# Kernel optimization log

Hardware: AMD Instinct MI355X
Metric: run time of the kernel (lower is better)

The kernel has to match this reference:

```python
import jax, jax.numpy as jnp
import numpy as np

B, T, V, E, U = 1024, 256, 50000, 512, 1024

def setup_inputs() -> dict:
    key = jax.random.key(0)
    ks = jax.random.split(key, 10)
    s = lambda k, shape, fan: jax.random.normal(k, shape, dtype=jnp.float32) * (1.0 / np.sqrt(fan))
    return {
        "inputs": jax.random.randint(ks[0], (B, T), 0, V, dtype=jnp.int32),
        "emb": s(ks[1], (V, E), E),
        "W0": s(ks[2], (E, U), E),
        "U0": s(ks[3], (U, U), U),
        "b0": jnp.zeros((U,), jnp.float32),
        "W1": s(ks[4], (U, U), U),
        "U1": s(ks[5], (U, U), U),
        "b1": jnp.zeros((U,), jnp.float32),
        "Wout": s(ks[6], (U, 1), U),
        "bout": jnp.zeros((1,), jnp.float32),
    }

def reference(inputs, emb, W0, U0, b0, W1, U1, b1, Wout, bout):
    x = emb[inputs]                      # [B, T, E] embedding lookup
    xT = jnp.swapaxes(x, 0, 1)           # [T, B, E] time-major for scan
    h0_init = jnp.zeros((inputs.shape[0], U0.shape[0]), x.dtype)
    h1_init = jnp.zeros((inputs.shape[0], U1.shape[0]), x.dtype)

    def step(carry, xt):
        h0, h1 = carry
        h0 = jnp.tanh(xt @ W0 + h0 @ U0 + b0)   # SimpleRNNCell 0 (dropout inactive, inference)
        h1 = jnp.tanh(h0 @ W1 + h1 @ U1 + b1)   # SimpleRNNCell 1
        return (h0, h1), None

    (h0, h1), _ = jax.lax.scan(step, (h0_init, h1_init), xT)
    return jax.nn.sigmoid(h1 @ Wout + bout)      # [B, 1]
```

## Files before the change

### kernel.cpp

```cpp
#include <hip/hip_runtime.h>
#include <hip/hip_cooperative_groups.h>
#include <math.h>

namespace cg = cooperative_groups;

typedef unsigned short u16;
typedef __bf16 bf16x8 __attribute__((ext_vector_type(8)));
typedef float f32x4 __attribute__((ext_vector_type(4)));
typedef unsigned short u16x8 __attribute__((ext_vector_type(8)));
typedef int i32x4 __attribute__((ext_vector_type(4)));

#define NBLK 256
#define NTHR 256
#define BB 1024
#define TT 256
#define EE 512
#define UU 1024
#define K0 1536
#define K1 2048
#define NK0 48
#define NK1 64
#define HN0 ((size_t)BB * K0)
#define HN1 ((size_t)BB * K1)
#define LDS_BYTES 131072

#define ROSTER_BASE 0
#define FLAG_BASE 32
#define EPOCH_BASE (32 + 2048)
#define BAR_INTS 2560

#define AUX_SC0 1

__device__ i32x4 llvm_amdgcn_raw_buffer_load_i32x4(i32x4 srsrc, int voffset, int soffset,
                                                   int aux) __asm("llvm.amdgcn.raw.buffer.load.v4i32");

__device__ __forceinline__ i32x4 make_srd(const void* p) {
  union { const void* p; int i[2]; } u; u.p = p;
  i32x4 r; r.x = u.i[0]; r.y = u.i[1]; r.z = -1; r.w = 0x00020000;
  return r;
}

__device__ __forceinline__ u16 f2bf(float f) {
  unsigned u = __builtin_bit_cast(unsigned, f);
  u += 0x7fffu + ((u >> 16) & 1u);
  return (u16)(u >> 16);
}
__device__ __forceinline__ float bf2f(u16 h) {
  return __builtin_bit_cast(float, ((unsigned)h) << 16);
}
__device__ __forceinline__ float fast_tanh(float x) {
  x = fminf(fmaxf(x, -15.f), 15.f);
  float e = __expf(2.f * x);
  return (e - 1.f) / (e + 1.f);
}

template<int K, int KLOW>
__device__ __forceinline__ void wfill(u16* __restrict__ Wt,
    const float* __restrict__ Wl, const float* __restrict__ Wh, int gstart) {
  constexpr int NK = K / 32;
  constexpr int NG = 1024 * K / 8;
  for (int g = gstart; g < NG; g += NBLK * NTHR) {
    const int lane = g & 63;
    const int r = g >> 6;
    const int kt = r % NK;
    const int cb = r / NK;
    const int n = cb * 16 + (lane & 15);
    const int kb = kt * 32 + (lane >> 4) * 8;
    u16x8 o;
#pragma unroll
    for (int e = 0; e < 8; ++e) {
      const int k = kb + e;
      const float v = (k < KLOW) ? Wl[(size_t)k * UU + n] : Wh[(size_t)(k - KLOW) * UU + n];
      o[e] = f2bf(v);
    }
    *(u16x8*)(Wt + (size_t)g * 8) = o;
  }
}

__device__ __forceinline__ void xbar(int* __restrict__ bar, int xcc, int slot, int nx,
                                     int tgt, int tid) {
  __syncthreads();
  if (tid < 64) {
    if (tid == 0)
      __hip_atomic_store(&bar[FLAG_BASE + xcc * 256 + slot], tgt,
                         __ATOMIC_RELAXED, __HIP_MEMORY_SCOPE_AGENT);
    if (slot == 0) {
      for (int base = 0; base < nx; base += 64) {
        const int i = base + tid;
        const bool act = (i < nx);
        int guard = 0;
        bool done = false;
        do {
          int v = act ? __hip_atomic_load(&bar[FLAG_BASE + xcc * 256 + i],
                                          __ATOMIC_RELAXED, __HIP_MEMORY_SCOPE_AGENT)
                      : tgt;
          done = __all(v >= tgt) != 0;
        } while (!done && ++guard < 300000);
      }
      if (tid == 0)
        __hip_atomic_store(&bar[EPOCH_BASE + xcc * 32], tgt,
                           __ATOMIC_RELAXED, __HIP_MEMORY_SCOPE_AGENT);
    } else if (tid == 0) {
      int guard = 0;
      while (__hip_atomic_load(&bar[EPOCH_BASE + xcc * 32],
                               __ATOMIC_RELAXED, __HIP_MEMORY_SCOPE_AGENT) < tgt
             && ++guard < 600000)
        __builtin_amdgcn_s_sleep(8);
    }
  }
  __syncthreads();
}

template<int K>
__device__ __forceinline__ void gemm2(const i32x4& srdA, int voA,
    const u16* __restrict__ bA, const u16* __restrict__ bB, int lane,
    f32x4 (&acc)[2][4]) {
  constexpr int NK = K / 32;
#pragma unroll 4
  for (int kt = 0; kt < NK; ++kt) {
    i32x4 a0 = llvm_amdgcn_raw_buffer_load_i32x4(srdA, voA + kt * 64, 0, AUX_SC0);
    i32x4 a1 = llvm_amdgcn_raw_buffer_load_i32x4(srdA, voA + 16 * K * 2 + kt * 64, 0, AUX_SC0);
    u16x8 b0 = *(const u16x8*)(bA + (size_t)(0 * NK + kt) * 512 + lane * 8);
    u16x8 b1 = *(const u16x8*)(bA + (size_t)(1 * NK + kt) * 512 + lane * 8);
    u16x8 b2 = *(const u16x8*)(bB + (size_t)(0 * NK + kt) * 512 + lane * 8);
    u16x8 b3 = *(const u16x8*)(bB + (size_t)(1 * NK + kt) * 512 + lane * 8);
    bf16x8 fa0 = __builtin_bit_cast(bf16x8, a0);
    bf16x8 fa1 = __builtin_bit_cast(bf16x8, a1);
    bf16x8 fb0 = __builtin_bit_cast(bf16x8, b0);
    bf16x8 fb1 = __builtin_bit_cast(bf16x8, b1);
    bf16x8 fb2 = __builtin_bit_cast(bf16x8, b2);
    bf16x8 fb3 = __builtin_bit_cast(bf16x8, b3);
    acc[0][0] = __builtin_amdgcn_mfma_f32_16x16x32_bf16(fa0, fb0, acc[0][0], 0, 0, 0);
    acc[0][1] = __builtin_amdgcn_mfma_f32_16x16x32_bf16(fa0, fb1, acc[0][1], 0, 0, 0);
    acc[0][2] = __builtin_amdgcn_mfma_f32_16x16x32_bf16(fa0, fb2, acc[0][2], 0, 0, 0);
    acc[0][3] = __builtin_amdgcn_mfma_f32_16x16x32_bf16(fa0, fb3, acc[0][3], 0, 0, 0);
    acc[1][0] = __builtin_amdgcn_mfma_f32_16x16x32_bf16(fa1, fb0, acc[1][0], 0, 0, 0);
    acc[1][1] = __builtin_amdgcn_mfma_f32_16x16x32_bf16(fa1, fb1, acc[1][1], 0, 0, 0);
    acc[1][2] = __builtin_amdgcn_mfma_f32_16x16x32_bf16(fa1, fb2, acc[1][2], 0, 0, 0);
    acc[1][3] = __builtin_amdgcn_mfma_f32_16x16x32_bf16(fa1, fb3, acc[1][3], 0, 0, 0);
  }
}

__device__ __forceinline__ void do_l0(int tk, int xcc, int jl, bool uselds,
    const u16* __restrict__ ldsb, const u16* __restrict__ Wt0,
    const int* __restrict__ inputs, const float* __restrict__ emb,
    const float* __restrict__ b0, u16* __restrict__ A0, u16* __restrict__ A1,
    int tid)
{
  const int lane = tid & 63, w = tid >> 6, q = lane >> 4, l16 = lane & 15;
  const int c0 = jl * 64;
  if (tk < TT - 1) {
    const int grow = xcc * 128 + jl * 8 + (tid >> 5);
    const int c = (tid & 31) * 16;
    const int idx = inputs[grow * TT + tk + 1];
    const f32x4* s = (const f32x4*)(emb + (size_t)idx * EE + c);
    f32x4 f0 = s[0], f1 = s[1], f2 = s[2], f3 = s[3];
    u16x8 oa, ob;
#pragma unroll
    for (int j = 0; j < 4; ++j) {
      oa[j] = f2bf(f0[j]); oa[j + 4] = f2bf(f1[j]);
      ob[j] = f2bf(f2[j]); ob[j + 4] = f2bf(f3[j]);
    }
    u16* dst = A0 + (size_t)((tk + 1) & 1) * HN0 + (size_t)grow * K0 + c;
    *(u16x8*)dst = oa;
    *(u16x8*)(dst + 8) = ob;
  }
  if (tk < TT) {
    f32x4 acc[2][4];
#pragma unroll
    for (int i = 0; i < 2; ++i)
#pragma unroll
      for (int n = 0; n < 4; ++n) acc[i][n] = (f32x4){0.f, 0.f, 0.f, 0.f};
    i32x4 srdA = make_srd(A0 + (size_t)(tk & 1) * HN0);
    const int voA = ((xcc * 128 + w * 32 + l16) * K0 + q * 8) * 2;
    const u16* bB = Wt0 + (size_t)(c0 / 16 + 2) * NK0 * 512;
    if (uselds) gemm2<K0>(srdA, voA, ldsb, bB, lane, acc);
    else        gemm2<K0>(srdA, voA, Wt0 + (size_t)(c0 / 16) * NK0 * 512, bB, lane, acc);
    u16* d1 = A1 + (size_t)(tk & 1) * HN1;
    u16* d2 = A0 + (size_t)((tk + 1) & 1) * HN0 + 512;
#pragma unroll
    for (int n = 0; n < 4; ++n) {
      const int col = c0 + n * 16 + l16;
      const float bs = b0[col];
#pragma unroll
      for (int i = 0; i < 2; ++i) {
#pragma unroll
        for (int rr = 0; rr < 4; ++rr) {
          const int grow = xcc * 128 + w * 32 + i * 16 + q * 4 + rr;
          const u16 v = f2bf(fast_tanh(acc[i][n][rr] + bs));
          d1[(size_t)grow * K1 + col] = v;
          d2[(size_t)grow * K0 + col] = v;
        }
      }
    }
  }
}

__device__ __forceinline__ void do_l1(int tk, int xcc, int jl, bool uselds,
    const u16* __restrict__ ldsb, const u16* __restrict__ Wt1,
    const float* __restrict__ b1, u16* __restrict__ A1, int tid)
{
  const int lane = tid & 63, w = tid >> 6, q = lane >> 4, l16 = lane & 15;
  const int c0 = jl * 64;
  f32x4 acc[2][4];
#pragma unroll
  for (int i = 0; i < 2; ++i)
#pragma unroll
    for (int n = 0; n < 4; ++n) acc[i][n] = (f32x4){0.f, 0.f, 0.f, 0.f};
  i32x4 srdA = make_srd(A1 + (size_t)((tk - 1) & 1) * HN1);
  const int voA = ((xcc * 128 + w * 32 + l16) * K1 + q * 8) * 2;
  const u16* bB = Wt1 + (size_t)(c0 / 16 + 2) * NK1 * 512;
  if (uselds) gemm2<K1>(srdA, voA, ldsb, bB, lane, acc);
  else        gemm2<K1>(srdA, voA, Wt1 + (size_t)(c0 / 16) * NK1 * 512, bB, lane, acc);
  u16* d1 = A1 + (size_t)(tk & 1) * HN1 + 1024;
#pragma unroll
  for (int n = 0; n < 4; ++n) {
    const int col = c0 + n * 16 + l16;
    const float bs = b1[col];
#pragma unroll
    for (int i = 0; i < 2; ++i) {
#pragma unroll
      for (int rr = 0; rr < 4; ++rr) {
        const int grow = xcc * 128 + w * 32 + i * 16 + q * 4 + rr;
        d1[(size_t)grow * K1 + col] = f2bf(fast_tanh(acc[i][n][rr] + bs));
      }
    }
  }
}

__global__ __launch_bounds__(NTHR, 1)
void rnn_kernel(const int* __restrict__ inputs, const float* __restrict__ emb,
    const float* __restrict__ W0, const float* __restrict__ U0, const float* __restrict__ b0,
    const float* __restrict__ W1, const float* __restrict__ U1, const float* __restrict__ b1,
    const float* __restrict__ Wout, const float* __restrict__ bout,
    float* __restrict__ out,
    u16* __restrict__ Wt0, u16* __restrict__ Wt1,
    u16* __restrict__ A0, u16* __restrict__ A1, int* __restrict__ bar)
{
  extern __shared__ u16 lds[];
  int* li = (int*)lds;
  cg::grid_group grid = cg::this_grid();
  const int tid = threadIdx.x, bid = blockIdx.x;

  const int gstart = bid * NTHR + tid;
  wfill<K0, 512>(Wt0, W0, U0, gstart);
  wfill<K1, 1024>(Wt1, W1, U1, gstart);
  for (int g = gstart; g < BB * EE / 8; g += NBLK * NTHR) {
    const int b = g >> 6, seg = g & 63;
    const int idx = inputs[b * TT];
    const f32x4* s = (const f32x4*)(emb + (size_t)idx * EE + seg * 8);
    f32x4 f0 = s[0], f1 = s[1];
    u16x8 o;
#pragma unroll
    for (int j = 0; j < 4; ++j) { o[j] = f2bf(f0[j]); o[j + 4] = f2bf(f1[j]); }
    *(u16x8*)(A0 + (size_t)b * K0 + seg * 8) = o;
  }
  {
    const u16x8 z = {0, 0, 0, 0, 0, 0, 0, 0};
    for (int g = gstart; g < BB * 1024 / 8; g += NBLK * NTHR) {
      const int b = g >> 7, seg = g & 127;
      *(u16x8*)(A0 + (size_t)b * K0 + 512 + seg * 8) = z;
      *(u16x8*)(A1 + (size_t)b * K1 + 1024 + seg * 8) = z;
    }
  }
  if (bid == 0) for (int i = tid; i < BAR_INTS; i += NTHR) bar[i] = 0;
  grid.sync();

  if (tid == 0) {
    const int xc = __builtin_amdgcn_s_getreg((7 << 11) | 20) & 7;
    li[0] = xc;
    li[1] = atomicAdd(&bar[ROSTER_BASE + xc], 1);
  }
  __syncthreads();
  const int xcc = li[0], slot = li[1];
  __syncthreads();
  grid.sync();
  if (tid == 0)
    li[0] = __hip_atomic_load(&bar[ROSTER_BASE + xcc],
                              __ATOMIC_RELAXED, __HIP_MEMORY_SCOPE_AGENT);
  __syncthreads();
  const int nx = li[0];
  __syncthreads();

  if (slot < 32) {
    const bool pL0 = slot < 16;
    const int cb = (pL0 ? slot : slot - 16) * 4;
    const int NKp = pL0 ? NK0 : NK1;
    const u16x8* s = (const u16x8*)((pL0 ? Wt0 : Wt1) + (size_t)cb * NKp * 512);
    const int nv = 2 * NKp * 64;
    u16x8* d = (u16x8*)lds;
    for (int i = tid; i < nv; i += NTHR) d[i] = s[i];
  }
  __syncthreads();

  for (int tk = 0; tk <= TT; ++tk) {
    for (int job = slot; job < 32; job += nx) {
      const bool uselds = (job == slot);
      if (job < 16) do_l0(tk, xcc, job, uselds, lds, Wt0, inputs, emb, b0, A0, A1, tid);
      else if (tk >= 1) do_l1(tk, xcc, job - 16, uselds, lds, Wt1, b1, A1, tid);
    }
    xbar(bar, xcc, slot, nx, tk + 1, tid);
  }

  if (slot == 0) {
    const int lane = tid & 63, w = tid >> 6;
    i32x4 srdH = make_srd(A1);
    const f32x4* wv = (const f32x4*)(Wout + lane * 16);
    f32x4 w0 = wv[0], w1 = wv[1], w2 = wv[2], w3 = wv[3];
    for (int rr = 0; rr < 32; ++rr) {
      const int grow = xcc * 128 + w * 32 + rr;
      const int vo = (grow * K1 + 1024 + lane * 16) * 2;
      i32x4 hv0 = llvm_amdgcn_raw_buffer_load_i32x4(srdH, vo, 0, AUX_SC0);
      i32x4 hv1 = llvm_amdgcn_raw_buffer_load_i32x4(srdH, vo + 16, 0, AUX_SC0);
      u16x8 lo = __builtin_bit_cast(u16x8, hv0);
      u16x8 hi = __builtin_bit_cast(u16x8, hv1);
      float s = 0.f;
#pragma unroll
      for (int j = 0; j < 4; ++j) {
        s += bf2f(lo[j]) * w0[j];
        s += bf2f(lo[j + 4]) * w1[j];
        s += bf2f(hi[j]) * w2[j];
        s += bf2f(hi[j + 4]) * w3[j];
      }
#pragma unroll
      for (int off = 32; off > 0; off >>= 1) s += __shfl_down(s, off);
      if (lane == 0) out[grow] = 1.f / (1.f + expf(-(s + bout[0])));
    }
  }
}

extern "C" void kernel_launch(void* const* d_in, const int* in_sizes, int n_in,
                              void* d_out, int out_size, void* d_ws, size_t ws_size,
                              hipStream_t stream)
{
  (void)in_sizes; (void)n_in; (void)out_size; (void)ws_size;
  const int*   inputs = (const int*)d_in[0];
  const float* emb    = (const float*)d_in[1];
  const float* W0     = (const float*)d_in[2];
  const float* U0     = (const float*)d_in[3];
  const float* b0     = (const float*)d_in[4];
  const float* W1     = (const float*)d_in[5];
  const float* U1     = (const float*)d_in[6];
  const float* b1     = (const float*)d_in[7];
  const float* Wout   = (const float*)d_in[8];
  const float* bout   = (const float*)d_in[9];
  float* out = (float*)d_out;

  u16* Wt0 = (u16*)d_ws;
  u16* Wt1 = Wt0 + (size_t)1024 * K0;
  u16* A0  = Wt1 + (size_t)1024 * K1;
  u16* A1  = A0 + (size_t)2 * 1024 * K0;
  int* bar = (int*)(A1 + (size_t)2 * 1024 * K1);

  static int lds_set = 0;
  if (!lds_set) {
    hipFuncSetAttribute((const void*)rnn_kernel,
                        hipFuncAttributeMaxDynamicSharedMemorySize, LDS_BYTES);
    lds_set = 1;
  }

  void* args[] = { &inputs, &emb, &W0, &U0, &b0, &W1, &U1, &b1, &Wout, &bout,
                   &out, &Wt0, &Wt1, &A0, &A1, &bar };
  hipLaunchCooperativeKernel((void*)rnn_kernel, dim3(NBLK), dim3(NTHR), args, LDS_BYTES, stream);
}
```

Baseline: 7.367 ms.

## Split K across two wave teams per block and software-pipeline operand loads

Doubles threads per block to 512 and splits each tile's K loop between two 256-thread teams. The second team writes its partial accumulators to a new LDS region, and the first team reduces them and applies bias and tanh. The GEMM inner loop now prefetches operands three k-steps ahead to hide global and LDS latency, and the embedding load is overlapped with the GEMM. In exchange it adds two block barriers per job, more LDS, and tighter register limits from launch_bounds(512,2).

```diff
diff --git a/kernel.cpp b/kernel.cpp
--- a/kernel.cpp
+++ b/kernel.cpp
@@ -11,7 +11,7 @@
 typedef int i32x4 __attribute__((ext_vector_type(4)));
 
 #define NBLK 256
-#define NTHR 256
+#define NTHR 512
 #define BB 1024
 #define TT 256
 #define EE 512
@@ -22,7 +22,7 @@
 #define NK1 64
 #define HN0 ((size_t)BB * K0)
 #define HN1 ((size_t)BB * K1)
-#define LDS_BYTES 131072
+#define LDS_BYTES 163840
 
 #define ROSTER_BASE 0
 #define FLAG_BASE 32
@@ -111,59 +111,79 @@
   __syncthreads();
 }
 
+struct Ops { i32x4 a0, a1; u16x8 b0, b1, b2, b3; };
+
+template<int K>
+__device__ __forceinline__ Ops ld_ops(const i32x4& srdA, int voA,
+    const u16* __restrict__ bA, const u16* __restrict__ bB, int lo, int kt) {
+  constexpr int NK = K / 32;
+  Ops o;
+  o.a0 = llvm_amdgcn_raw_buffer_load_i32x4(srdA, voA + kt * 64, 0, AUX_SC0);
+  o.a1 = llvm_amdgcn_raw_buffer_load_i32x4(srdA, voA + 16 * K * 2 + kt * 64, 0, AUX_SC0);
+  o.b0 = *(const u16x8*)(bA + (size_t)kt * 512 + lo);
+  o.b1 = *(const u16x8*)(bA + (size_t)(NK + kt) * 512 + lo);
+  o.b2 = *(const u16x8*)(bB + (size_t)kt * 512 + lo);
+  o.b3 = *(const u16x8*)(bB + (size_t)(NK + kt) * 512 + lo);
+  return o;
+}
+
+__device__ __forceinline__ void mfma8(const Ops& o, f32x4 (&acc)[2][4]) {
+  bf16x8 fa0 = __builtin_bit_cast(bf16x8, o.a0);
+  bf16x8 fa1 = __builtin_bit_cast(bf16x8, o.a1);
+  bf16x8 fb0 = __builtin_bit_cast(bf16x8, o.b0);
+  bf16x8 fb1 = __builtin_bit_cast(bf16x8, o.b1);
+  bf16x8 fb2 = __builtin_bit_cast(bf16x8, o.b2);
+  bf16x8 fb3 = __builtin_bit_cast(bf16x8, o.b3);
+  acc[0][0] = __builtin_amdgcn_mfma_f32_16x16x32_bf16(fa0, fb0, acc[0][0], 0, 0, 0);
+  acc[0][1] = __builtin_amdgcn_mfma_f32_16x16x32_bf16(fa0, fb1, acc[0][1], 0, 0, 0);
+  acc[0][2] = __builtin_amdgcn_mfma_f32_16x16x32_bf16(fa0, fb2, acc[0][2], 0, 0, 0);
+  acc[0][3] = __builtin_amdgcn_mfma_f32_16x16x32_bf16(fa0, fb3, acc[0][3], 0, 0, 0);
+  acc[1][0] = __builtin_amdgcn_mfma_f32_16x16x32_bf16(fa1, fb0, acc[1][0], 0, 0, 0);
+  acc[1][1] = __builtin_amdgcn_mfma_f32_16x16x32_bf16(fa1, fb1, acc[1][1], 0, 0, 0);
+  acc[1][2] = __builtin_amdgcn_mfma_f32_16x16x32_bf16(fa1, fb2, acc[1][2], 0, 0, 0);
+  acc[1][3] = __builtin_amdgcn_mfma_f32_16x16x32_bf16(fa1, fb3, acc[1][3], 0, 0, 0);
+}
+
 template<int K>
 __device__ __forceinline__ void gemm2(const i32x4& srdA, int voA,
     const u16* __restrict__ bA, const u16* __restrict__ bB, int lane,
-    f32x4 (&acc)[2][4]) {
-  constexpr int NK = K / 32;
+    int kt0, int ktn, f32x4 (&acc)[2][4]) {
+  const int lo = lane * 8;
+  Ops q0 = ld_ops<K>(srdA, voA, bA, bB, lo, kt0);
+  Ops q1 = ld_ops<K>(srdA, voA, bA, bB, lo, kt0 + 1);
+  Ops q2 = ld_ops<K>(srdA, voA, bA, bB, lo, kt0 + 2);
 #pragma unroll 4
-  for (int kt = 0; kt < NK; ++kt) {
-    i32x4 a0 = llvm_amdgcn_raw_buffer_load_i32x4(srdA, voA + kt * 64, 0, AUX_SC0);
-    i32x4 a1 = llvm_amdgcn_raw_buffer_load_i32x4(srdA, voA + 16 * K * 2 + kt * 64, 0, AUX_SC0);
-    u16x8 b0 = *(const u16x8*)(bA + (size_t)(0 * NK + kt) * 512 + lane * 8);
-    u16x8 b1 = *(const u16x8*)(bA + (size_t)(1 * NK + kt) * 512 + lane * 8);
-    u16x8 b2 = *(const u16x8*)(bB + (size_t)(0 * NK + kt) * 512 + lane * 8);
-    u16x8 b3 = *(const u16x8*)(bB + (size_t)(1 * NK + kt) * 512 + lane * 8);
-    bf16x8 fa0 = __builtin_bit_cast(bf16x8, a0);
-    bf16x8 fa1 = __builtin_bit_cast(bf16x8, a1);
-    bf16x8 fb0 = __builtin_bit_cast(bf16x8, b0);
-    bf16x8 fb1 = __builtin_bit_cast(bf16x8, b1);
-    bf16x8 fb2 = __builtin_bit_cast(bf16x8, b2);
-    bf16x8 fb3 = __builtin_bit_cast(bf16x8, b3);
-    acc[0][0] = __builtin_amdgcn_mfma_f32_16x16x32_bf16(fa0, fb0, acc[0][0], 0, 0, 0);
-    acc[0][1] = __builtin_amdgcn_mfma_f32_16x16x32_bf16(fa0, fb1, acc[0][1], 0, 0, 0);
-    acc[0][2] = __builtin_amdgcn_mfma_f32_16x16x32_bf16(fa0, fb2, acc[0][2], 0, 0, 0);
-    acc[0][3] = __builtin_amdgcn_mfma_f32_16x16x32_bf16(fa0, fb3, acc[0][3], 0, 0, 0);
-    acc[1][0] = __builtin_amdgcn_mfma_f32_16x16x32_bf16(fa1, fb0, acc[1][0], 0, 0, 0);
-    acc[1][1] = __builtin_amdgcn_mfma_f32_16x16x32_bf16(fa1, fb1, acc[1][1], 0, 0, 0);
-    acc[1][2] = __builtin_amdgcn_mfma_f32_16x16x32_bf16(fa1, fb2, acc[1][2], 0, 0, 0);
-    acc[1][3] = __builtin_amdgcn_mfma_f32_16x16x32_bf16(fa1, fb3, acc[1][3], 0, 0, 0);
-  }
+  for (int kt = kt0; kt < ktn - 3; ++kt) {
+    Ops q3 = ld_ops<K>(srdA, voA, bA, bB, lo, kt + 3);
+    mfma8(q0, acc);
+    q0 = q1; q1 = q2; q2 = q3;
+  }
+  mfma8(q0, acc);
+  mfma8(q1, acc);
+  mfma8(q2, acc);
 }
 
 __device__ __forceinline__ void do_l0(int tk, int xcc, int jl, bool uselds,
-    const u16* __restrict__ ldsb, const u16* __restrict__ Wt0,
+    u16* ldsm, const u16* __restrict__ Wt0,
     const int* __restrict__ inputs, const float* __restrict__ emb,
     const float* __restrict__ b0, u16* __restrict__ A0, u16* __restrict__ A1,
     int tid)
 {
-  const int lane = tid & 63, w = tid >> 6, q = lane >> 4, l16 = lane & 15;
+  const int lane = tid & 63, wv = (tid >> 6) & 3, q = lane >> 4, l16 = lane & 15;
+  const int team = tid >> 8;
+  const int ltid = tid & 255;
   const int c0 = jl * 64;
-  if (tk < TT - 1) {
-    const int grow = xcc * 128 + jl * 8 + (tid >> 5);
-    const int c = (tid & 31) * 16;
-    const int idx = inputs[grow * TT + tk + 1];
-    const f32x4* s = (const f32x4*)(emb + (size_t)idx * EE + c);
-    f32x4 f0 = s[0], f1 = s[1], f2 = s[2], f3 = s[3];
-    u16x8 oa, ob;
-#pragma unroll
-    for (int j = 0; j < 4; ++j) {
-      oa[j] = f2bf(f0[j]); oa[j + 4] = f2bf(f1[j]);
-      ob[j] = f2bf(f2[j]); ob[j + 4] = f2bf(f3[j]);
-    }
-    u16* dst = A0 + (size_t)((tk + 1) & 1) * HN0 + (size_t)grow * K0 + c;
-    *(u16x8*)dst = oa;
-    *(u16x8*)(dst + 8) = ob;
+  f32x4* part = (f32x4*)(ldsm + 65536);
+
+  f32x4 f0, f1;
+  int egrow = 0, ec = 0;
+  const bool do_emb = (tk < TT - 1);
+  if (do_emb) {
+    egrow = xcc * 128 + jl * 8 + (tid >> 6);
+    ec = (tid & 63) * 8;
+    const int idx = inputs[egrow * TT + tk + 1];
+    const f32x4* s = (const f32x4*)(emb + (size_t)idx * EE + ec);
+    f0 = s[0]; f1 = s[1];
   }
   if (tk < TT) {
     f32x4 acc[2][4];
@@ -172,63 +192,104 @@
 #pragma unroll
       for (int n = 0; n < 4; ++n) acc[i][n] = (f32x4){0.f, 0.f, 0.f, 0.f};
     i32x4 srdA = make_srd(A0 + (size_t)(tk & 1) * HN0);
-    const int voA = ((xcc * 128 + w * 32 + l16) * K0 + q * 8) * 2;
+    const int voA = ((xcc * 128 + wv * 32 + l16) * K0 + q * 8) * 2;
+    const int kt0 = team * (NK0 / 2), ktn = kt0 + NK0 / 2;
     const u16* bB = Wt0 + (size_t)(c0 / 16 + 2) * NK0 * 512;
-    if (uselds) gemm2<K0>(srdA, voA, ldsb, bB, lane, acc);
-    else        gemm2<K0>(srdA, voA, Wt0 + (size_t)(c0 / 16) * NK0 * 512, bB, lane, acc);
-    u16* d1 = A1 + (size_t)(tk & 1) * HN1;
-    u16* d2 = A0 + (size_t)((tk + 1) & 1) * HN0 + 512;
+    const u16* bA = uselds ? (const u16*)ldsm
+                           : Wt0 + (size_t)(c0 / 16) * NK0 * 512;
+    gemm2<K0>(srdA, voA, bA, bB, lane, kt0, ktn, acc);
+    if (do_emb) {
+      u16x8 oa;
+#pragma unroll
+      for (int j = 0; j < 4; ++j) { oa[j] = f2bf(f0[j]); oa[j + 4] = f2bf(f1[j]); }
+      *(u16x8*)(A0 + (size_t)((tk + 1) & 1) * HN0 + (size_t)egrow * K0 + ec) = oa;
+    }
+    if (team) {
+#pragma unroll
+      for (int i = 0; i < 2; ++i)
+#pragma unroll
+        for (int n = 0; n < 4; ++n) part[(i * 4 + n) * 256 + ltid] = acc[i][n];
+    }
+    __syncthreads();
+    if (!team) {
+      u16* d1 = A1 + (size_t)(tk & 1) * HN1;
+      u16* d2 = A0 + (size_t)((tk + 1) & 1) * HN0 + 512;
+#pragma unroll
+      for (int i = 0; i < 2; ++i)
+#pragma unroll
+        for (int n = 0; n < 4; ++n) acc[i][n] += part[(i * 4 + n) * 256 + ltid];
+#pragma unroll
+      for (int n = 0; n < 4; ++n) {
+        const int col = c0 + n * 16 + l16;
+        const float bs = b0[col];
+#pragma unroll
+        for (int i = 0; i < 2; ++i) {
+#pragma unroll
+          for (int rr = 0; rr < 4; ++rr) {
+            const int grow = xcc * 128 + wv * 32 + i * 16 + q * 4 + rr;
+            const u16 v = f2bf(fast_tanh(acc[i][n][rr] + bs));
+            d1[(size_t)grow * K1 + col] = v;
+            d2[(size_t)grow * K0 + col] = v;
+          }
+        }
+      }
+    }
+    __syncthreads();
+  }
+}
+
+__device__ __forceinline__ void do_l1(int tk, int xcc, int jl, bool uselds,
+    u16* ldsm, const u16* __restrict__ Wt1,
+    const float* __restrict__ b1, u16* __restrict__ A1, int tid)
+{
+  const int lane = tid & 63, wv = (tid >> 6) & 3, q = lane >> 4, l16 = lane & 15;
+  const int team = tid >> 8;
+  const int ltid = tid & 255;
+  const int c0 = jl * 64;
+  f32x4* part = (f32x4*)(ldsm + 65536);
+  f32x4 acc[2][4];
+#pragma unroll
+  for (int i = 0; i < 2; ++i)
+#pragma unroll
+    for (int n = 0; n < 4; ++n) acc[i][n] = (f32x4){0.f, 0.f, 0.f, 0.f};
+  i32x4 srdA = make_srd(A1 + (size_t)((tk - 1) & 1) * HN1);
+  const int voA = ((xcc * 128 + wv * 32 + l16) * K1 + q * 8) * 2;
+  const int kt0 = team * (NK1 / 2), ktn = kt0 + NK1 / 2;
+  const u16* bB = Wt1 + (size_t)(c0 / 16 + 2) * NK1 * 512;
+  const u16* bA = uselds ? (const u16*)ldsm
+                         : Wt1 + (size_t)(c0 / 16) * NK1 * 512;
+  gemm2<K1>(srdA, voA, bA, bB, lane, kt0, ktn, acc);
+  if (team) {
+#pragma unroll
+    for (int i = 0; i < 2; ++i)
+#pragma unroll
+      for (int n = 0; n < 4; ++n) part[(i * 4 + n) * 256 + ltid] = acc[i][n];
+  }
+  __syncthreads();
+  if (!team) {
+    u16* d1 = A1 + (size_t)(tk & 1) * HN1 + 1024;
+#pragma unroll
+    for (int i = 0; i < 2; ++i)
+#pragma unroll
+      for (int n = 0; n < 4; ++n) acc[i][n] += part[(i * 4 + n) * 256 + ltid];
 #pragma unroll
     for (int n = 0; n < 4; ++n) {
       const int col = c0 + n * 16 + l16;
-      const float bs = b0[col];
+      const float bs = b1[col];
 #pragma unroll
       for (int i = 0; i < 2; ++i) {
 #pragma unroll
         for (int rr = 0; rr < 4; ++rr) {
-          const int grow = xcc * 128 + w * 32 + i * 16 + q * 4 + rr;
-          const u16 v = f2bf(fast_tanh(acc[i][n][rr] + bs));
-          d1[(size_t)grow * K1 + col] = v;
-          d2[(size_t)grow * K0 + col] = v;
+          const int grow = xcc * 128 + wv * 32 + i * 16 + q * 4 + rr;
+          d1[(size_t)grow * K1 + col] = f2bf(fast_tanh(acc[i][n][rr] + bs));
         }
       }
     }
   }
-}
-
-__device__ __forceinline__ void do_l1(int tk, int xcc, int jl, bool uselds,
-    const u16* __restrict__ ldsb, const u16* __restrict__ Wt1,
-    const float* __restrict__ b1, u16* __restrict__ A1, int tid)
-{
-  const int lane = tid & 63, w = tid >> 6, q = lane >> 4, l16 = lane & 15;
-  const int c0 = jl * 64;
-  f32x4 acc[2][4];
-#pragma unroll
-  for (int i = 0; i < 2; ++i)
-#pragma unroll
-    for (int n = 0; n < 4; ++n) acc[i][n] = (f32x4){0.f, 0.f, 0.f, 0.f};
-  i32x4 srdA = make_srd(A1 + (size_t)((tk - 1) & 1) * HN1);
-  const int voA = ((xcc * 128 + w * 32 + l16) * K1 + q * 8) * 2;
-  const u16* bB = Wt1 + (size_t)(c0 / 16 + 2) * NK1 * 512;
-  if (uselds) gemm2<K1>(srdA, voA, ldsb, bB, lane, acc);
-  else        gemm2<K1>(srdA, voA, Wt1 + (size_t)(c0 / 16) * NK1 * 512, bB, lane, acc);
-  u16* d1 = A1 + (size_t)(tk & 1) * HN1 + 1024;
-#pragma unroll
-  for (int n = 0; n < 4; ++n) {
-    const int col = c0 + n * 16 + l16;
-    const float bs = b1[col];
-#pragma unroll
-    for (int i = 0; i < 2; ++i) {
-#pragma unroll
-      for (int rr = 0; rr < 4; ++rr) {
-        const int grow = xcc * 128 + w * 32 + i * 16 + q * 4 + rr;
-        d1[(size_t)grow * K1 + col] = f2bf(fast_tanh(acc[i][n][rr] + bs));
-      }
-    }
-  }
-}
-
-__global__ __launch_bounds__(NTHR, 1)
+  __syncthreads();
+}
+
+__global__ __launch_bounds__(NTHR, 2)
 void rnn_kernel(const int* __restrict__ inputs, const float* __restrict__ emb,
     const float* __restrict__ W0, const float* __restrict__ U0, const float* __restrict__ b0,
     const float* __restrict__ W1, const float* __restrict__ U1, const float* __restrict__ b1,
@@ -307,8 +368,8 @@
     i32x4 srdH = make_srd(A1);
     const f32x4* wv = (const f32x4*)(Wout + lane * 16);
     f32x4 w0 = wv[0], w1 = wv[1], w2 = wv[2], w3 = wv[3];
-    for (int rr = 0; rr < 32; ++rr) {
-      const int grow = xcc * 128 + w * 32 + rr;
+    for (int rr = 0; rr < 16; ++rr) {
+      const int grow = xcc * 128 + w * 16 + rr;
       const int vo = (grow * K1 + 1024 + lane * 16) * 2;
       i32x4 hv0 = llvm_amdgcn_raw_buffer_load_i32x4(srdH, vo, 0, AUX_SC0);
       i32x4 hv1 = llvm_amdgcn_raw_buffer_load_i32x4(srdH, vo + 16, 0, AUX_SC0);
```

New measurement: 8.556 ms. 16.1% more time.
